# Performance work log

Measured on AMD Instinct MI355X. Metric: run time of the kernel, lower is better.

## Reference

```python
import jax, jax.numpy as jnp
import numpy as np

PI2 = 6.283185307


def setup_inputs() -> dict:
    key = jax.random.key(0)
    k1, k2, k3, k4 = jax.random.split(key, 4)
    T, n_mix, n_dim = 262144, 64, 16
    data = jax.random.normal(k1, (T, n_dim), dtype=jnp.float32)
    # mixture weights: positive, roughly summing to 1
    wghts = jax.random.uniform(k2, (n_mix, 1), dtype=jnp.float32, minval=0.5, maxval=1.5) / n_mix
    means = jax.random.normal(k3, (n_mix, n_dim), dtype=jnp.float32)
    # diagonal covariances: strictly positive
    dcovs = jax.random.uniform(k4, (n_mix, n_dim), dtype=jnp.float32, minval=0.5, maxval=1.5)
    return {"data": data, "wghts": wghts, "means": means, "dcovs": dcovs}


def reference(data, wghts, means, dcovs):
    # data: (T, D); wghts: (M, 1); means: (M, D); dcovs: (M, D)
    n_dim = data.shape[1]
    c = 1.0 / np.sqrt(PI2 ** n_dim)  # Gaussian normalizer (2*pi)^{-D/2}
    c_dets = 1.0 / jnp.sqrt(jnp.prod(dcovs, axis=1))  # (M,) |Sigma|^{-1/2}
    dprecs = 1.0 / dcovs  # (M, D) diagonal precisions
    diff = data[:, None, :] - means[None, :, :]  # (T, M, D)
    mhbs_dist = jnp.einsum('tmd,md->tm', diff * diff, dprecs)  # (T, M)
    probs = (wghts[:, 0] * c * c_dets)[None, :] * jnp.exp(-0.5 * mhbs_dist)  # (T, M)
    likes = jnp.sum(probs, axis=1)  # (T,)
    log_likes = jnp.mean(jnp.log(likes))
    posteriors = probs / likes[:, None]  # (T, M)
    e_means = posteriors @ means  # (T, D) weighted mean of component means
    return (log_likes, e_means)
```

## Files before the change

### kernel.cpp

```cpp
#include <hip/hip_runtime.h>

#define T_TOTAL 262144
#define NBLOCKS 2048
#define NMIX 64
#define NDIM 16

typedef short bf16x8 __attribute__((ext_vector_type(8)));
typedef unsigned short u16x8 __attribute__((ext_vector_type(8)));
typedef unsigned short u16x4 __attribute__((ext_vector_type(4)));
typedef float f32x4 __attribute__((ext_vector_type(4)));

__device__ __forceinline__ unsigned short f2bf(float f) {
    union { float f; unsigned u; } v; v.f = f;
    unsigned r = v.u + 0x7fff + ((v.u >> 16) & 1);
    return (unsigned short)(r >> 16);
}
__device__ __forceinline__ float bf2f(unsigned short s) {
    union { unsigned u; float f; } v; v.u = ((unsigned)s) << 16;
    return v.f;
}

#define L_WH   0
#define L_WL   5120
#define L_MUT  10240
#define L_A2   12544
#define L_RED  12800
#define L_F    12864
#define L_P    31296

__global__ __launch_bounds__(256, 4) void gmm_main(const float* __restrict__ data,
                                                   const float* __restrict__ wghts,
                                                   const float* __restrict__ means,
                                                   const float* __restrict__ dcovs,
                                                   float* __restrict__ out,
                                                   float* __restrict__ part) {
    __shared__ __align__(16) char lds[40512];
    const int tid  = threadIdx.x;
    const int w    = tid >> 6;
    const int lane = tid & 63;
    const int gi   = lane & 15;
    const int gq   = lane >> 4;
    const size_t tblk = (size_t)blockIdx.x * 128;

    const int row = tid >> 1, half = tid & 1;
    const float4* xp = (const float4*)(data + (tblk + row) * 16 + half * 8);
    float4 xa = xp[0], xb = xp[1];

    {
        const int m  = tid >> 2;
        const int ql = tid & 3;
        const float LOG2E = 1.4426950408889634f;
        const float LOG2_2PI = 2.6514961294723187f;
        const float4 d4 = *(const float4*)(dcovs + m * 16 + ql * 4);
        const float4 m4 = *(const float4*)(means + m * 16 + ql * 4);
        const float wm = wghts[m];
        float dc[4] = {d4.x, d4.y, d4.z, d4.w};
        float mu[4] = {m4.x, m4.y, m4.z, m4.w};
        u16x4 ghv, glv, hhv, hlv;
        float sumlog = 0.0f, qsum = 0.0f;
        unsigned short* mut = (unsigned short*)(lds + L_MUT);
#pragma unroll
        for (int j = 0; j < 4; ++j) {
            float pr = __builtin_amdgcn_rcpf(dc[j]);
            float g = -0.5f * LOG2E * pr;
            float h = LOG2E * pr * mu[j];
            unsigned short gH = f2bf(g), hH = f2bf(h);
            ghv[j] = gH;  glv[j] = f2bf(g - bf2f(gH));
            hhv[j] = hH;  hlv[j] = f2bf(h - bf2f(hH));
            mut[(ql * 4 + j) * 72 + m] = f2bf(mu[j]);
            sumlog += __builtin_amdgcn_logf(dc[j]);
            qsum   += pr * mu[j] * mu[j];
        }
        char* wrh = lds + L_WH + m * 80;
        char* wrl = lds + L_WL + m * 80;
        *(u16x4*)(wrh + ql * 8)      = ghv;
        *(u16x4*)(wrh + 32 + ql * 8) = hhv;
        *(u16x4*)(wrl + ql * 8)      = glv;
        *(u16x4*)(wrl + 32 + ql * 8) = hlv;
        sumlog += __shfl_xor(sumlog, 1); sumlog += __shfl_xor(sumlog, 2);
        qsum   += __shfl_xor(qsum, 1);   qsum   += __shfl_xor(qsum, 2);
        if (ql == 0) {
            float log2C = __builtin_amdgcn_logf(wm) - 8.0f * LOG2_2PI - 0.5f * sumlog;
            ((float*)(lds + L_A2))[m] = log2C - 0.5f * LOG2E * qsum;
        }
    }

    {
        int fw = row >> 5, lr = row & 31;
        float xv[8] = {xa.x, xa.y, xa.z, xa.w, xb.x, xb.y, xb.z, xb.w};
        u16x8 vh2, vl2, vhx, vlx;
#pragma unroll
        for (int d = 0; d < 8; ++d) {
            float q = xv[d] * xv[d];
            unsigned short qh = f2bf(q);
            vh2[d] = qh;               vl2[d] = f2bf(q - bf2f(qh));
            unsigned short xh = f2bf(xv[d]);
            vhx[d] = xh;               vlx[d] = f2bf(xv[d] - bf2f(xh));
        }
        char* fb = lds + L_F + fw * 4608 + lr * 144;
        *(u16x8*)(fb + half * 16)        = vh2;
        *(u16x8*)(fb + 32 + half * 16)   = vhx;
        *(u16x8*)(fb + 64 + half * 16)   = vl2;
        *(u16x8*)(fb + 96 + half * 16)   = vlx;
    }
    __syncthreads();

    bf16x8 bh[4], bl[4];
    float a2v[4];
#pragma unroll
    for (int c = 0; c < 4; ++c) {
        bh[c] = *(const bf16x8*)(lds + L_WH + (c * 16 + gi) * 80 + gq * 16);
        bl[c] = *(const bf16x8*)(lds + L_WL + (c * 16 + gi) * 80 + gq * 16);
        a2v[c] = ((const float*)(lds + L_A2))[c * 16 + gi];
    }
    bf16x8 mf0 = *(const bf16x8*)(lds + L_MUT + gi * 144 + gq * 16);
    bf16x8 mf1 = *(const bf16x8*)(lds + L_MUT + gi * 144 + 64 + gq * 16);

    const char* fbase = lds + L_F + w * 4608;
    char* pbase = lds + L_P + w * 2304;
    float ll_acc = 0.0f;

#pragma unroll
    for (int rt = 0; rt < 2; ++rt) {
        bf16x8 ah = *(const bf16x8*)(fbase + (rt * 16 + gi) * 144 + gq * 16);
        bf16x8 al = *(const bf16x8*)(fbase + (rt * 16 + gi) * 144 + 64 + gq * 16);

        f32x4 pacc[4];
#pragma unroll
        for (int c = 0; c < 4; ++c) {
            f32x4 a = {0.0f, 0.0f, 0.0f, 0.0f};
            a = __builtin_amdgcn_mfma_f32_16x16x32_bf16(al, bh[c], a, 0, 0, 0);
            a = __builtin_amdgcn_mfma_f32_16x16x32_bf16(ah, bl[c], a, 0, 0, 0);
            a = __builtin_amdgcn_mfma_f32_16x16x32_bf16(ah, bh[c], a, 0, 0, 0);
            pacc[c] = a;
        }

        float p[4][4], prow[4], inv[4];
#pragma unroll
        for (int reg = 0; reg < 4; ++reg) {
#pragma unroll
            for (int c = 0; c < 4; ++c)
                p[c][reg] = __builtin_amdgcn_exp2f(pacc[c][reg] + a2v[c]);
            prow[reg] = (p[0][reg] + p[1][reg]) + (p[2][reg] + p[3][reg]);
        }
#pragma unroll
        for (int reg = 0; reg < 4; ++reg) {
            float v = prow[reg];
            v += __shfl_xor(v, 1);  v += __shfl_xor(v, 2);
            v += __shfl_xor(v, 4);  v += __shfl_xor(v, 8);
            v = fmaxf(v, 1e-35f);
            ll_acc += __builtin_amdgcn_logf(v);
            inv[reg] = __builtin_amdgcn_rcpf(v);
        }

#pragma unroll
        for (int c = 0; c < 4; ++c)
#pragma unroll
            for (int reg = 0; reg < 4; ++reg)
                *(unsigned short*)(pbase + (gq * 4 + reg) * 144 + (c * 16 + gi) * 2) =
                    f2bf(p[c][reg]);

        bf16x8 ap0 = *(const bf16x8*)(pbase + gi * 144 + gq * 16);
        bf16x8 ap1 = *(const bf16x8*)(pbase + gi * 144 + 64 + gq * 16);
        f32x4 e = {0.0f, 0.0f, 0.0f, 0.0f};
        e = __builtin_amdgcn_mfma_f32_16x16x32_bf16(ap0, mf0, e, 0, 0, 0);
        e = __builtin_amdgcn_mfma_f32_16x16x32_bf16(ap1, mf1, e, 0, 0, 0);

        size_t trow = tblk + (size_t)w * 32 + rt * 16 + gq * 4;
#pragma unroll
        for (int reg = 0; reg < 4; ++reg)
            out[1 + (trow + reg) * 16 + gi] = e[reg] * inv[reg];
    }

    ll_acc += __shfl_xor(ll_acc, 16);
    ll_acc += __shfl_xor(ll_acc, 32);
    if (lane == 0) ((float*)(lds + L_RED))[w] = ll_acc;
    __syncthreads();
    if (tid == 0) {
        float* r = (float*)(lds + L_RED);
        part[blockIdx.x] = (r[0] + r[1]) + (r[2] + r[3]);
    }
}

__global__ void gmm_fin(const float* __restrict__ part, float* __restrict__ out) {
    __shared__ double red[4];
    const int tid = threadIdx.x;
    double s = 0.0;
#pragma unroll
    for (int k = 0; k < 8; ++k) s += (double)part[tid + k * 256];
#pragma unroll
    for (int off = 32; off > 0; off >>= 1) s += __shfl_down(s, off, 64);
    const int wv = tid >> 6, lane = tid & 63;
    if (lane == 0) red[wv] = s;
    __syncthreads();
    if (tid == 0) {
        const double LN2 = 0.6931471805599453;
        double tot = (red[0] + red[1]) + (red[2] + red[3]);
        out[0] = (float)(tot * LN2 / (double)T_TOTAL);
    }
}

extern "C" void kernel_launch(void* const* d_in, const int* in_sizes, int n_in,
                              void* d_out, int out_size, void* d_ws, size_t ws_size,
                              hipStream_t stream) {
    const float* data  = (const float*)d_in[0];
    const float* wghts = (const float*)d_in[1];
    const float* means = (const float*)d_in[2];
    const float* dcovs = (const float*)d_in[3];
    float* out  = (float*)d_out;
    float* part = (float*)d_ws;

    gmm_main<<<NBLOCKS, 256, 0, stream>>>(data, wghts, means, dcovs, out, part);
    gmm_fin<<<1, 256, 0, stream>>>(part, out);
}
```

Before: 85.37 us.

## Build MFMA A-fragments from registers and double rows per block

Result: no change. 85.81 us (+0.5%).

```diff
diff --git a/kernel.cpp b/kernel.cpp
--- a/kernel.cpp
+++ b/kernel.cpp
@@ -1,7 +1,7 @@
 #include <hip/hip_runtime.h>
 
 #define T_TOTAL 262144
-#define NBLOCKS 2048
+#define NBLOCKS 1024
 #define NMIX 64
 #define NDIM 16
 
@@ -25,8 +25,7 @@
 #define L_MUT  10240
 #define L_A2   12544
 #define L_RED  12800
-#define L_F    12864
-#define L_P    31296
+#define L_P    12864
 
 __global__ __launch_bounds__(256, 4) void gmm_main(const float* __restrict__ data,
                                                    const float* __restrict__ wghts,
@@ -34,17 +33,24 @@
                                                    const float* __restrict__ dcovs,
                                                    float* __restrict__ out,
                                                    float* __restrict__ part) {
-    __shared__ __align__(16) char lds[40512];
+    __shared__ __align__(16) char lds[22080];
     const int tid  = threadIdx.x;
     const int w    = tid >> 6;
     const int lane = tid & 63;
     const int gi   = lane & 15;
     const int gq   = lane >> 4;
-    const size_t tblk = (size_t)blockIdx.x * 128;
-
-    const int row = tid >> 1, half = tid & 1;
-    const float4* xp = (const float4*)(data + (tblk + row) * 16 + half * 8);
-    float4 xa = xp[0], xb = xp[1];
+    const size_t tblk = (size_t)blockIdx.x * 256;
+
+    float4 xva[4], xvb[4];
+    {
+        const float* base = data + (tblk + w * 64 + gi) * 16 + (gq & 1) * 8;
+#pragma unroll
+        for (int rt = 0; rt < 4; ++rt) {
+            const float4* xp = (const float4*)(base + rt * 16 * 16);
+            xva[rt] = xp[0];
+            xvb[rt] = xp[1];
+        }
+    }
 
     {
         const int m  = tid >> 2;
@@ -84,25 +90,6 @@
             ((float*)(lds + L_A2))[m] = log2C - 0.5f * LOG2E * qsum;
         }
     }
-
-    {
-        int fw = row >> 5, lr = row & 31;
-        float xv[8] = {xa.x, xa.y, xa.z, xa.w, xb.x, xb.y, xb.z, xb.w};
-        u16x8 vh2, vl2, vhx, vlx;
-#pragma unroll
-        for (int d = 0; d < 8; ++d) {
-            float q = xv[d] * xv[d];
-            unsigned short qh = f2bf(q);
-            vh2[d] = qh;               vl2[d] = f2bf(q - bf2f(qh));
-            unsigned short xh = f2bf(xv[d]);
-            vhx[d] = xh;               vlx[d] = f2bf(xv[d] - bf2f(xh));
-        }
-        char* fb = lds + L_F + fw * 4608 + lr * 144;
-        *(u16x8*)(fb + half * 16)        = vh2;
-        *(u16x8*)(fb + 32 + half * 16)   = vhx;
-        *(u16x8*)(fb + 64 + half * 16)   = vl2;
-        *(u16x8*)(fb + 96 + half * 16)   = vlx;
-    }
     __syncthreads();
 
     bf16x8 bh[4], bl[4];
@@ -116,14 +103,23 @@
     bf16x8 mf0 = *(const bf16x8*)(lds + L_MUT + gi * 144 + gq * 16);
     bf16x8 mf1 = *(const bf16x8*)(lds + L_MUT + gi * 144 + 64 + gq * 16);
 
-    const char* fbase = lds + L_F + w * 4608;
     char* pbase = lds + L_P + w * 2304;
     float ll_acc = 0.0f;
-
-#pragma unroll
-    for (int rt = 0; rt < 2; ++rt) {
-        bf16x8 ah = *(const bf16x8*)(fbase + (rt * 16 + gi) * 144 + gq * 16);
-        bf16x8 al = *(const bf16x8*)(fbase + (rt * 16 + gi) * 144 + 64 + gq * 16);
+    const bool sq = (gq < 2);
+
+#pragma unroll
+    for (int rt = 0; rt < 4; ++rt) {
+        float4 a4 = xva[rt], b4 = xvb[rt];
+        float xv[8] = {a4.x, a4.y, a4.z, a4.w, b4.x, b4.y, b4.z, b4.w};
+        u16x8 ahv, alv;
+#pragma unroll
+        for (int d = 0; d < 8; ++d) {
+            float v = sq ? xv[d] * xv[d] : xv[d];
+            unsigned short vh = f2bf(v);
+            ahv[d] = vh;
+            alv[d] = f2bf(v - bf2f(vh));
+        }
+        bf16x8 ah = (bf16x8)ahv, al = (bf16x8)alv;
 
         f32x4 pacc[4];
 #pragma unroll
@@ -166,7 +162,7 @@
         e = __builtin_amdgcn_mfma_f32_16x16x32_bf16(ap0, mf0, e, 0, 0, 0);
         e = __builtin_amdgcn_mfma_f32_16x16x32_bf16(ap1, mf1, e, 0, 0, 0);
 
-        size_t trow = tblk + (size_t)w * 32 + rt * 16 + gq * 4;
+        size_t trow = tblk + (size_t)w * 64 + rt * 16 + gq * 4;
 #pragma unroll
         for (int reg = 0; reg < 4; ++reg)
             out[1 + (trow + reg) * 16 + gi] = e[reg] * inv[reg];
@@ -187,7 +183,7 @@
     const int tid = threadIdx.x;
     double s = 0.0;
 #pragma unroll
-    for (int k = 0; k < 8; ++k) s += (double)part[tid + k * 256];
+    for (int k = 0; k < 4; ++k) s += (double)part[tid + k * 256];
 #pragma unroll
     for (int off = 32; off > 0; off >>= 1) s += __shfl_down(s, off, 64);
     const int wv = tid >> 6, lane = tid & 63;
```
